# Performance work log

Hardware: AMD Instinct MI355X
Metric: run time of the kernel (lower is better)

## Reference

```python
import jax, jax.numpy as jnp
import numpy as np

NUM_EXPERTS = 8
TOP_K = 2
D_MODEL = 1024
EXPERT_CAP = 512  # dim_feedforward // num_experts = 4096 // 8
B, S = 4, 2048


def setup_inputs() -> dict:
    key = jax.random.key(0)
    ks = jax.random.split(key, 4)
    scale = 1.0 / np.sqrt(D_MODEL)
    x = jax.random.normal(ks[0], (B, S, D_MODEL), dtype=jnp.float32)
    gate_w = jax.random.normal(ks[1], (D_MODEL, NUM_EXPERTS), dtype=jnp.float32) * scale
    w1 = jax.random.normal(ks[2], (NUM_EXPERTS, D_MODEL, EXPERT_CAP), dtype=jnp.float32) * scale
    b1 = jnp.zeros((NUM_EXPERTS, EXPERT_CAP), dtype=jnp.float32)
    w2 = jax.random.normal(ks[3], (NUM_EXPERTS, EXPERT_CAP, D_MODEL), dtype=jnp.float32) * (1.0 / np.sqrt(EXPERT_CAP))
    b2 = jnp.zeros((NUM_EXPERTS, D_MODEL), dtype=jnp.float32)
    return {"x": x, "gate_w": gate_w, "w1": w1, "b1": b1, "w2": w2, "b2": b2}


def reference(x, gate_w, w1, b1, w2, b2):
    Bx, Sx, D = x.shape
    xt = x.reshape(-1, D)  # [N, D], N = B*S
    gates = jax.nn.softmax(xt @ gate_w, axis=-1)           # [N, E]
    topk_g, topk_i = jax.lax.top_k(gates, TOP_K)           # [N, K]
    # Faithful to source: every selected expert is scaled by the SUM of all top-k gates
    tok_w = topk_g.sum(axis=-1)                            # [N]
    sel = (topk_i[:, :, None] == jnp.arange(NUM_EXPERTS)[None, None, :]).any(axis=1)  # [N, E] bool
    # Dense per-expert MLP (E small), then mask-combine (scatter-add equivalent)
    h = jax.nn.gelu(jnp.einsum('nd,edh->enh', xt, w1) + b1[:, None, :], approximate=False)  # [E, N, H]
    y = jnp.einsum('enh,ehd->end', h, w2) + b2[:, None, :]  # [E, N, D]
    out = jnp.einsum('end,ne,n->nd', y, sel.astype(x.dtype), tok_w)  # [N, D]
    return out.reshape(Bx, Sx, D)
```

## Files before the change

### kernel.cpp

```cpp
#include <hip/hip_runtime.h>
#include <math.h>

#define N_TOK 8192
#define DM 1024
#define NE 8
#define HE 512
#define NPAIR 16384
#define MAXMB 264

#define BM 64
#define BN 128
#define BK 64

#define GSTR 1028

typedef __bf16 bf16x8 __attribute__((ext_vector_type(8)));
typedef float f32x4 __attribute__((ext_vector_type(4)));

#define GLOBAL_AS __attribute__((address_space(1)))
#define LDS_AS    __attribute__((address_space(3)))

__device__ __forceinline__ void gl_lds16(const void* g, void* lds) {
    __builtin_amdgcn_global_load_lds((const GLOBAL_AS unsigned int*)g,
                                     (LDS_AS unsigned int*)lds, 16, 0, 0);
}

__device__ __forceinline__ unsigned short f2bf(float f) {
    unsigned int u = __float_as_uint(f);
    u += 0x7fffu + ((u >> 16) & 1u);
    return (unsigned short)(u >> 16);
}

__device__ __forceinline__ float bf2f(unsigned short u) {
    return __uint_as_float(((unsigned int)u) << 16);
}

__device__ __forceinline__ float gelu_exact(float v) {
    return 0.5f * v * (1.0f + erff(v * 0.70710678118654752440f));
}

__device__ __forceinline__ double shfl_xor_dbl(double v, int m) {
    long long l = __double_as_longlong(v);
    int lo = (int)(l & 0xffffffffll);
    int hi = (int)(l >> 32);
    lo = __shfl_xor(lo, m, 64);
    hi = __shfl_xor(hi, m, 64);
    return __longlong_as_double(((long long)hi << 32) | (unsigned long long)(unsigned int)lo);
}

__global__ void transpose_cast2_kernel(const float* __restrict__ w1,
                                       const float* __restrict__ w2,
                                       unsigned short* __restrict__ w1t,
                                       unsigned short* __restrict__ w2t) {
    __shared__ float tile[64][65];
    int z = blockIdx.z;
    const float* src; unsigned short* dst; int R, C, c0, r0;
    if (z < 8) {
        src = w1 + (size_t)z * DM * HE; dst = w1t + (size_t)z * DM * HE;
        R = DM; C = HE; c0 = blockIdx.x * 64; r0 = blockIdx.y * 64;
    } else {
        int e = z - 8;
        src = w2 + (size_t)e * HE * DM; dst = w2t + (size_t)e * HE * DM;
        R = HE; C = DM; c0 = blockIdx.y * 64; r0 = blockIdx.x * 64;
    }
    int tc = threadIdx.x & 63, tg = threadIdx.x >> 6;
    #pragma unroll
    for (int i = 0; i < 16; i++) {
        int r = tg * 16 + i;
        tile[r][tc] = src[(size_t)(r0 + r) * C + (c0 + tc)];
    }
    __syncthreads();
    #pragma unroll
    for (int i = 0; i < 16; i++) {
        int r = tg * 16 + i;
        dst[(size_t)(c0 + r) * R + (r0 + tc)] = f2bf(tile[tc][r]);
    }
}

__global__ __launch_bounds__(256) void gate_cast_kernel(
        const float* __restrict__ x, const float* __restrict__ gw,
        unsigned short* __restrict__ xb,
        float* __restrict__ w_tok, int* __restrict__ e_sel) {
    __shared__ float gls[NE * GSTR];
    int tid = threadIdx.x;
    for (int v = tid; v < 2048; v += 256) {
        float4 g4 = ((const float4*)gw)[v];
        int idx = v * 4;
        int d = idx >> 3;
        int e0 = idx & 7;
        gls[(e0    ) * GSTR + d] = g4.x;
        gls[(e0 + 1) * GSTR + d] = g4.y;
        gls[(e0 + 2) * GSTR + d] = g4.z;
        gls[(e0 + 3) * GSTR + d] = g4.w;
    }
    __syncthreads();

    int n = blockIdx.x * 4 + (tid >> 6);
    int lane = tid & 63;
    const float4* xr = (const float4*)(x + (size_t)n * DM);
    ushort4* xw = (ushort4*)(xb + (size_t)n * DM);

    double s[NE];
    #pragma unroll
    for (int e = 0; e < NE; e++) s[e] = 0.0;

    #pragma unroll
    for (int i = 0; i < 4; i++) {
        float4 x4 = xr[i * 64 + lane];
        ushort4 o;
        o.x = f2bf(x4.x); o.y = f2bf(x4.y); o.z = f2bf(x4.z); o.w = f2bf(x4.w);
        xw[i * 64 + lane] = o;
        int d = (i * 64 + lane) * 4;
        #pragma unroll
        for (int e = 0; e < NE; e++) {
            float4 g4 = *(const float4*)(&gls[e * GSTR + d]);
            s[e] += (double)x4.x * (double)g4.x + (double)x4.y * (double)g4.y
                  + (double)x4.z * (double)g4.z + (double)x4.w * (double)g4.w;
        }
    }
    #pragma unroll
    for (int e = 0; e < NE; e++) {
        for (int off = 32; off > 0; off >>= 1)
            s[e] += shfl_xor_dbl(s[e], off);
    }
    if (lane == 0) {
        double m = s[0];
        for (int e = 1; e < NE; e++) if (s[e] > m) m = s[e];
        double sum = 0.0;
        for (int e = 0; e < NE; e++) sum += exp(s[e] - m);
        int i1 = 0; double v1 = s[0];
        for (int e = 1; e < NE; e++) if (s[e] > v1) { v1 = s[e]; i1 = e; }
        int i2 = -1; double v2 = -1e300;
        for (int e = 0; e < NE; e++) if (e != i1 && s[e] > v2) { v2 = s[e]; i2 = e; }
        w_tok[n] = (float)((exp(v1 - m) + exp(v2 - m)) / sum);
        e_sel[2 * n]     = i1;
        e_sel[2 * n + 1] = i2;
    }
}

__global__ __launch_bounds__(1024) void route_kernel(
        const int* __restrict__ e_sel, int* __restrict__ cnt, int* __restrict__ offs,
        int* __restrict__ pair_tok, int* __restrict__ slotmap,
        int* __restrict__ mb_e, int* __restrict__ mb_base, int* __restrict__ n_mb) {
    __shared__ int wbin[16][NE];
    __shared__ int wstart[16][NE];
    __shared__ int etot[NE], eoffs[NE], bofs[NE];
    int tid = threadIdx.x;
    int w = tid >> 6, l = tid & 63;
    if (l < NE) wbin[w][l] = 0;
    __syncthreads();

    int sel[16];
    #pragma unroll
    for (int k = 0; k < 16; k++) {
        sel[k] = e_sel[tid * 16 + k];
        atomicAdd(&wbin[w][sel[k]], 1);
    }
    __syncthreads();

    if (tid < NE) {
        int t = 0;
        for (int ww = 0; ww < 16; ww++) t += wbin[ww][tid];
        etot[tid] = t;
    }
    __syncthreads();
    if (tid == 0) {
        int a = 0, b = 0;
        for (int e = 0; e < NE; e++) {
            eoffs[e] = a; a += etot[e];
            bofs[e] = b;  b += (etot[e] + BM - 1) / BM;
        }
        n_mb[0] = b;
    }
    __syncthreads();
    if (tid < NE) {
        cnt[tid] = etot[tid];
        offs[tid] = eoffs[tid];
        int r = eoffs[tid];
        for (int ww = 0; ww < 16; ww++) { wstart[ww][tid] = r; r += wbin[ww][tid]; }
        int nb = (etot[tid] + BM - 1) / BM;
        int b0 = bofs[tid];
        for (int b = 0; b < nb; b++) {
            mb_e[b0 + b] = tid;
            mb_base[b0 + b] = eoffs[tid] + b * BM;
        }
    }
    __syncthreads();
    if (l < NE) wbin[w][l] = wstart[w][l];
    __syncthreads();

    #pragma unroll
    for (int k = 0; k < 16; k++) {
        int i = tid * 16 + k;
        int slot = atomicAdd(&wbin[w][sel[k]], 1);
        pair_tok[slot] = i >> 1;
        slotmap[i] = slot;
    }
}

__global__ __launch_bounds__(256, 4) void gemm1_kernel(
        const unsigned short* __restrict__ xb,
        const unsigned short* __restrict__ w1t,
        const float* __restrict__ b1,
        const int* __restrict__ pair_tok,
        const int* __restrict__ cnt, const int* __restrict__ offs,
        const int* __restrict__ mb_e, const int* __restrict__ mb_base,
        const int* __restrict__ n_mb,
        unsigned short* __restrict__ hbuf) {
    int mb = blockIdx.y;
    if (mb >= n_mb[0]) return;
    int e = mb_e[mb];
    int sbase = mb_base[mb];
    int vlim = offs[e] + cnt[e];
    int n0 = blockIdx.x * BN;

    __shared__ __align__(16) unsigned short As[BM * BK];
    __shared__ __align__(16) unsigned short Bs[BN * BK];

    int tid = threadIdx.x;
    int lane = tid & 63;
    int w = tid >> 6;
    int wu = __builtin_amdgcn_readfirstlane(w);
    int l3 = lane >> 3, l7 = lane & 7;
    int g = l7 ^ l3;

    const char* aptr[2];
    const char* bptr[4];
    #pragma unroll
    for (int j = 0; j < 2; j++) {
        int row = w * 16 + j * 8 + l3;
        int slot = sbase + row;
        int t = pair_tok[slot < vlim ? slot : vlim - 1];
        aptr[j] = (const char*)xb + (size_t)t * (DM * 2) + g * 16;
    }
    #pragma unroll
    for (int j = 0; j < 4; j++) {
        int row = w * 32 + j * 8 + l3;
        bptr[j] = (const char*)w1t + ((size_t)e * HE + n0 + row) * (DM * 2) + g * 16;
    }

    int wm = (w & 1) * 32;
    int wn = (w >> 1) * 64;
    int fr = lane & 15;
    int fq = lane >> 4;

    f32x4 acc[2][4];
    #pragma unroll
    for (int i = 0; i < 2; i++)
        #pragma unroll
        for (int j = 0; j < 4; j++)
            acc[i][j] = (f32x4){0.f, 0.f, 0.f, 0.f};

    for (int k0 = 0; k0 < DM; k0 += BK) {
        int kb = k0 * 2;
        #pragma unroll
        for (int j = 0; j < 2; j++)
            gl_lds16(aptr[j] + kb, (char*)As + wu * 2048 + j * 1024);
        #pragma unroll
        for (int j = 0; j < 4; j++)
            gl_lds16(bptr[j] + kb, (char*)Bs + wu * 4096 + j * 1024);
        __syncthreads();
        #pragma unroll
        for (int kk2 = 0; kk2 < 2; kk2++) {
            int sw = ((kk2 * 4 + fq) ^ (fr & 7)) << 4;
            bf16x8 af[2], bfv[4];
            #pragma unroll
            for (int i = 0; i < 2; i++)
                af[i] = *(const bf16x8*)((const char*)As + (wm + i * 16 + fr) * 128 + sw);
            #pragma unroll
            for (int j = 0; j < 4; j++)
                bfv[j] = *(const bf16x8*)((const char*)Bs + (wn + j * 16 + fr) * 128 + sw);
            #pragma unroll
            for (int i = 0; i < 2; i++)
                #pragma unroll
                for (int j = 0; j < 4; j++)
                    acc[i][j] = __builtin_amdgcn_mfma_f32_16x16x32_bf16(af[i], bfv[j], acc[i][j], 0, 0, 0);
        }
        __syncthreads();
    }

    #pragma unroll
    for (int j = 0; j < 4; j++) {
        int nn = n0 + wn + j * 16 + fr;
        float bias = b1[e * HE + nn];
        #pragma unroll
        for (int i = 0; i < 2; i++) {
            #pragma unroll
            for (int r = 0; r < 4; r++) {
                int mm = wm + i * 16 + fq * 4 + r;
                if (sbase + mm < vlim) {
                    float v = acc[i][j][r] + bias;
                    hbuf[(size_t)(sbase + mm) * HE + nn] = f2bf(gelu_exact(v));
                }
            }
        }
    }
}

__global__ __launch_bounds__(256, 4) void gemm2_kernel(
        const unsigned short* __restrict__ hbuf,
        const unsigned short* __restrict__ w2t,
        const float* __restrict__ b2,
        const int* __restrict__ pair_tok,
        const float* __restrict__ w_tok,
        const int* __restrict__ cnt, const int* __restrict__ offs,
        const int* __restrict__ mb_e, const int* __restrict__ mb_base,
        const int* __restrict__ n_mb,
        unsigned short* __restrict__ ybuf) {
    int mb = blockIdx.y;
    if (mb >= n_mb[0]) return;
    int e = mb_e[mb];
    int sbase = mb_base[mb];
    int vlim = offs[e] + cnt[e];
    int n0 = blockIdx.x * BN;

    __shared__ __align__(16) unsigned short As[BM * BK];
    __shared__ __align__(16) unsigned short Bs[BN * BK];
    __shared__ float wts[BM];

    int tid = threadIdx.x;
    if (tid < BM) {
        int slot = sbase + tid;
        wts[tid] = w_tok[pair_tok[slot < vlim ? slot : vlim - 1]];
    }
    __syncthreads();

    int lane = tid & 63;
    int w = tid >> 6;
    int wu = __builtin_amdgcn_readfirstlane(w);
    int l3 = lane >> 3, l7 = lane & 7;
    int g = l7 ^ l3;

    const char* aptr[2];
    const char* bptr[4];
    #pragma unroll
    for (int j = 0; j < 2; j++) {
        int row = w * 16 + j * 8 + l3;
        int slot = sbase + row;
        int cs = (slot < vlim) ? slot : vlim - 1;
        aptr[j] = (const char*)hbuf + (size_t)cs * (HE * 2) + g * 16;
    }
    #pragma unroll
    for (int j = 0; j < 4; j++) {
        int row = w * 32 + j * 8 + l3;
        bptr[j] = (const char*)w2t + ((size_t)e * DM + n0 + row) * (HE * 2) + g * 16;
    }

    int wm = (w & 1) * 32;
    int wn = (w >> 1) * 64;
    int fr = lane & 15;
    int fq = lane >> 4;

    f32x4 acc[2][4];
    #pragma unroll
    for (int i = 0; i < 2; i++)
        #pragma unroll
        for (int j = 0; j < 4; j++)
            acc[i][j] = (f32x4){0.f, 0.f, 0.f, 0.f};

    for (int k0 = 0; k0 < HE; k0 += BK) {
        int kb = k0 * 2;
        #pragma unroll
        for (int j = 0; j < 2; j++)
            gl_lds16(aptr[j] + kb, (char*)As + wu * 2048 + j * 1024);
        #pragma unroll
        for (int j = 0; j < 4; j++)
            gl_lds16(bptr[j] + kb, (char*)Bs + wu * 4096 + j * 1024);
        __syncthreads();
        #pragma unroll
        for (int kk2 = 0; kk2 < 2; kk2++) {
            int sw = ((kk2 * 4 + fq) ^ (fr & 7)) << 4;
            bf16x8 af[2], bfv[4];
            #pragma unroll
            for (int i = 0; i < 2; i++)
                af[i] = *(const bf16x8*)((const char*)As + (wm + i * 16 + fr) * 128 + sw);
            #pragma unroll
            for (int j = 0; j < 4; j++)
                bfv[j] = *(const bf16x8*)((const char*)Bs + (wn + j * 16 + fr) * 128 + sw);
            #pragma unroll
            for (int i = 0; i < 2; i++)
                #pragma unroll
                for (int j = 0; j < 4; j++)
                    acc[i][j] = __builtin_amdgcn_mfma_f32_16x16x32_bf16(af[i], bfv[j], acc[i][j], 0, 0, 0);
        }
        __syncthreads();
    }

    #pragma unroll
    for (int j = 0; j < 4; j++) {
        int dd = n0 + wn + j * 16 + fr;
        float bias = b2[e * DM + dd];
        #pragma unroll
        for (int i = 0; i < 2; i++) {
            #pragma unroll
            for (int r = 0; r < 4; r++) {
                int mm = wm + i * 16 + fq * 4 + r;
                if (sbase + mm < vlim) {
                    float wgt = wts[mm];
                    ybuf[(size_t)(sbase + mm) * DM + dd] = f2bf(wgt * (acc[i][j][r] + bias));
                }
            }
        }
    }
}

__global__ void combine_kernel(const unsigned short* __restrict__ yb,
                               const int* __restrict__ slotmap,
                               float* __restrict__ out) {
    int i = blockIdx.x * 256 + threadIdx.x;
    int n = i >> 8;
    int c = (i & 255) * 4;
    int s1 = slotmap[2 * n];
    int s2 = slotmap[2 * n + 1];
    ushort4 a = *(const ushort4*)(&yb[(size_t)s1 * DM + c]);
    ushort4 b = *(const ushort4*)(&yb[(size_t)s2 * DM + c]);
    float4 o;
    o.x = bf2f(a.x) + bf2f(b.x);
    o.y = bf2f(a.y) + bf2f(b.y);
    o.z = bf2f(a.z) + bf2f(b.z);
    o.w = bf2f(a.w) + bf2f(b.w);
    ((float4*)out)[i] = o;
}

extern "C" void kernel_launch(void* const* d_in, const int* in_sizes, int n_in,
                              void* d_out, int out_size, void* d_ws, size_t ws_size,
                              hipStream_t stream) {
    const float* x  = (const float*)d_in[0];
    const float* gw = (const float*)d_in[1];
    const float* w1 = (const float*)d_in[2];
    const float* b1 = (const float*)d_in[3];
    const float* w2 = (const float*)d_in[4];
    const float* b2 = (const float*)d_in[5];
    float* out = (float*)d_out;

    char* ws = (char*)d_ws;
    unsigned short* ybuf = (unsigned short*)(ws);
    unsigned short* xb   = (unsigned short*)(ws);
    unsigned short* w1t  = (unsigned short*)(ws + 16777216);
    unsigned short* w2t  = (unsigned short*)(ws + 33554432);
    unsigned short* hbuf = (unsigned short*)(ws + 41943040);
    float* w_tok         = (float*)(ws + 58720256);
    int*   e_sel         = (int*)(ws + 58753024);
    int*   slotmap       = (int*)(ws + 58818560);
    int*   cnt           = (int*)(ws + 58884096);
    int*   offs          = (int*)(ws + 58884128);
    int*   pair_tok      = (int*)(ws + 58884224);
    int*   mb_e          = (int*)(ws + 58949760);
    int*   mb_base       = (int*)(ws + 58950848);
    int*   n_mb          = (int*)(ws + 58951936);

    transpose_cast2_kernel<<<dim3(8, 16, 16), 256, 0, stream>>>(w1, w2, w1t, w2t);
    gate_cast_kernel<<<N_TOK / 4, 256, 0, stream>>>(x, gw, xb, w_tok, e_sel);
    route_kernel<<<1, 1024, 0, stream>>>(e_sel, cnt, offs, pair_tok, slotmap,
                                         mb_e, mb_base, n_mb);
    gemm1_kernel<<<dim3(HE / BN, MAXMB), 256, 0, stream>>>(
        xb, w1t, b1, pair_tok, cnt, offs, mb_e, mb_base, n_mb, hbuf);
    gemm2_kernel<<<dim3(DM / BN, MAXMB), 256, 0, stream>>>(
        hbuf, w2t, b2, pair_tok, w_tok, cnt, offs, mb_e, mb_base, n_mb, ybuf);
    combine_kernel<<<(N_TOK * DM / 4) / 256, 256, 0, stream>>>(ybuf, slotmap, out);
}
```

Before: 235.3 us.

## Merge prep kernels, stage GEMM epilogues through LDS, widen combine loads

Folds the weight transpose/cast and the gate/cast kernels into a single launch, so one launch overhead goes away and the two kinds of work can share the GPU. Both GEMM epilogues now write bf16 results into LDS and then store whole rows with 16-byte vector writes, replacing scattered 2-byte global stores. The combine kernel reads 8 bf16 per load instead of 4. The cost is an extra LDS round trip and barrier per tile, plus a merged kernel that uses the larger shared-memory allocation for every block.

```diff
diff --git a/kernel.cpp b/kernel.cpp
--- a/kernel.cpp
+++ b/kernel.cpp
@@ -11,6 +11,7 @@
 #define BM 64
 #define BN 128
 #define BK 64
+#define OSTR 136
 
 #define GSTR 1028
 
@@ -29,10 +30,6 @@
     unsigned int u = __float_as_uint(f);
     u += 0x7fffu + ((u >> 16) & 1u);
     return (unsigned short)(u >> 16);
-}
-
-__device__ __forceinline__ float bf2f(unsigned short u) {
-    return __uint_as_float(((unsigned int)u) << 16);
 }
 
 __device__ __forceinline__ float gelu_exact(float v) {
@@ -48,41 +45,47 @@
     return __longlong_as_double(((long long)hi << 32) | (unsigned long long)(unsigned int)lo);
 }
 
-__global__ void transpose_cast2_kernel(const float* __restrict__ w1,
-                                       const float* __restrict__ w2,
-                                       unsigned short* __restrict__ w1t,
-                                       unsigned short* __restrict__ w2t) {
-    __shared__ float tile[64][65];
-    int z = blockIdx.z;
-    const float* src; unsigned short* dst; int R, C, c0, r0;
-    if (z < 8) {
-        src = w1 + (size_t)z * DM * HE; dst = w1t + (size_t)z * DM * HE;
-        R = DM; C = HE; c0 = blockIdx.x * 64; r0 = blockIdx.y * 64;
-    } else {
-        int e = z - 8;
-        src = w2 + (size_t)e * HE * DM; dst = w2t + (size_t)e * HE * DM;
-        R = HE; C = DM; c0 = blockIdx.y * 64; r0 = blockIdx.x * 64;
-    }
-    int tc = threadIdx.x & 63, tg = threadIdx.x >> 6;
-    #pragma unroll
-    for (int i = 0; i < 16; i++) {
-        int r = tg * 16 + i;
-        tile[r][tc] = src[(size_t)(r0 + r) * C + (c0 + tc)];
-    }
-    __syncthreads();
-    #pragma unroll
-    for (int i = 0; i < 16; i++) {
-        int r = tg * 16 + i;
-        dst[(size_t)(c0 + r) * R + (r0 + tc)] = f2bf(tile[tc][r]);
-    }
-}
-
-__global__ __launch_bounds__(256) void gate_cast_kernel(
+__global__ __launch_bounds__(256) void prep_kernel(
         const float* __restrict__ x, const float* __restrict__ gw,
+        const float* __restrict__ w1, const float* __restrict__ w2,
         unsigned short* __restrict__ xb,
+        unsigned short* __restrict__ w1t, unsigned short* __restrict__ w2t,
         float* __restrict__ w_tok, int* __restrict__ e_sel) {
-    __shared__ float gls[NE * GSTR];
+    __shared__ float smf[NE * GSTR];
+    int bid = blockIdx.x;
     int tid = threadIdx.x;
+
+    if (bid >= 2048) {
+        int t = bid - 2048;
+        int z = t >> 7;
+        int idx = t & 127;
+        int bx = idx & 7, by = idx >> 3;
+        const float* src; unsigned short* dst; int R, C, c0, r0;
+        if (z < 8) {
+            src = w1 + (size_t)z * DM * HE; dst = w1t + (size_t)z * DM * HE;
+            R = DM; C = HE; c0 = bx * 64; r0 = by * 64;
+        } else {
+            int e = z - 8;
+            src = w2 + (size_t)e * HE * DM; dst = w2t + (size_t)e * HE * DM;
+            R = HE; C = DM; c0 = by * 64; r0 = bx * 64;
+        }
+        float (*tile)[65] = (float(*)[65])smf;
+        int tc = tid & 63, tg = tid >> 6;
+        #pragma unroll
+        for (int i = 0; i < 16; i++) {
+            int r = tg * 16 + i;
+            tile[r][tc] = src[(size_t)(r0 + r) * C + (c0 + tc)];
+        }
+        __syncthreads();
+        #pragma unroll
+        for (int i = 0; i < 16; i++) {
+            int r = tg * 16 + i;
+            dst[(size_t)(c0 + r) * R + (r0 + tc)] = f2bf(tile[tc][r]);
+        }
+        return;
+    }
+
+    float* gls = smf;
     for (int v = tid; v < 2048; v += 256) {
         float4 g4 = ((const float4*)gw)[v];
         int idx = v * 4;
@@ -95,7 +98,7 @@
     }
     __syncthreads();
 
-    int n = blockIdx.x * 4 + (tid >> 6);
+    int n = bid * 4 + (tid >> 6);
     int lane = tid & 63;
     const float4* xr = (const float4*)(x + (size_t)n * DM);
     ushort4* xw = (ushort4*)(xb + (size_t)n * DM);
@@ -214,8 +217,9 @@
     int vlim = offs[e] + cnt[e];
     int n0 = blockIdx.x * BN;
 
-    __shared__ __align__(16) unsigned short As[BM * BK];
-    __shared__ __align__(16) unsigned short Bs[BN * BK];
+    __shared__ __align__(16) unsigned short smem[BM * BK + BN * BK];
+    char* As = (char*)smem;
+    char* Bs = (char*)smem + 8192;
 
     int tid = threadIdx.x;
     int lane = tid & 63;
@@ -255,10 +259,10 @@
         int kb = k0 * 2;
         #pragma unroll
         for (int j = 0; j < 2; j++)
-            gl_lds16(aptr[j] + kb, (char*)As + wu * 2048 + j * 1024);
+            gl_lds16(aptr[j] + kb, As + wu * 2048 + j * 1024);
         #pragma unroll
         for (int j = 0; j < 4; j++)
-            gl_lds16(bptr[j] + kb, (char*)Bs + wu * 4096 + j * 1024);
+            gl_lds16(bptr[j] + kb, Bs + wu * 4096 + j * 1024);
         __syncthreads();
         #pragma unroll
         for (int kk2 = 0; kk2 < 2; kk2++) {
@@ -266,10 +270,10 @@
             bf16x8 af[2], bfv[4];
             #pragma unroll
             for (int i = 0; i < 2; i++)
-                af[i] = *(const bf16x8*)((const char*)As + (wm + i * 16 + fr) * 128 + sw);
+                af[i] = *(const bf16x8*)(As + (wm + i * 16 + fr) * 128 + sw);
             #pragma unroll
             for (int j = 0; j < 4; j++)
-                bfv[j] = *(const bf16x8*)((const char*)Bs + (wn + j * 16 + fr) * 128 + sw);
+                bfv[j] = *(const bf16x8*)(Bs + (wn + j * 16 + fr) * 128 + sw);
             #pragma unroll
             for (int i = 0; i < 2; i++)
                 #pragma unroll
@@ -279,21 +283,27 @@
         __syncthreads();
     }
 
+    unsigned short* ot = smem;
     #pragma unroll
     for (int j = 0; j < 4; j++) {
-        int nn = n0 + wn + j * 16 + fr;
-        float bias = b1[e * HE + nn];
+        int nl = wn + j * 16 + fr;
+        float bias = b1[e * HE + n0 + nl];
         #pragma unroll
         for (int i = 0; i < 2; i++) {
             #pragma unroll
             for (int r = 0; r < 4; r++) {
                 int mm = wm + i * 16 + fq * 4 + r;
-                if (sbase + mm < vlim) {
-                    float v = acc[i][j][r] + bias;
-                    hbuf[(size_t)(sbase + mm) * HE + nn] = f2bf(gelu_exact(v));
-                }
+                ot[mm * OSTR + nl] = f2bf(gelu_exact(acc[i][j][r] + bias));
             }
         }
+    }
+    __syncthreads();
+    int row = tid >> 2;
+    int c0 = (tid & 3) * 32;
+    if (sbase + row < vlim) {
+        const uint4* sp = (const uint4*)(ot + row * OSTR + c0);
+        uint4* dp = (uint4*)(hbuf + (size_t)(sbase + row) * HE + n0 + c0);
+        dp[0] = sp[0]; dp[1] = sp[1]; dp[2] = sp[2]; dp[3] = sp[3];
     }
 }
 
@@ -314,8 +324,9 @@
     int vlim = offs[e] + cnt[e];
     int n0 = blockIdx.x * BN;
 
-    __shared__ __align__(16) unsigned short As[BM * BK];
-    __shared__ __align__(16) unsigned short Bs[BN * BK];
+    __shared__ __align__(16) unsigned short smem[BM * BK + BN * BK];
+    char* As = (char*)smem;
+    char* Bs = (char*)smem + 8192;
     __shared__ float wts[BM];
 
     int tid = threadIdx.x;
@@ -362,10 +373,10 @@
         int kb = k0 * 2;
         #pragma unroll
         for (int j = 0; j < 2; j++)
-            gl_lds16(aptr[j] + kb, (char*)As + wu * 2048 + j * 1024);
+            gl_lds16(aptr[j] + kb, As + wu * 2048 + j * 1024);
         #pragma unroll
         for (int j = 0; j < 4; j++)
-            gl_lds16(bptr[j] + kb, (char*)Bs + wu * 4096 + j * 1024);
+            gl_lds16(bptr[j] + kb, Bs + wu * 4096 + j * 1024);
         __syncthreads();
         #pragma unroll
         for (int kk2 = 0; kk2 < 2; kk2++) {
@@ -373,10 +384,10 @@
             bf16x8 af[2], bfv[4];
             #pragma unroll
             for (int i = 0; i < 2; i++)
-                af[i] = *(const bf16x8*)((const char*)As + (wm + i * 16 + fr) * 128 + sw);
+                af[i] = *(const bf16x8*)(As + (wm + i * 16 + fr) * 128 + sw);
             #pragma unroll
             for (int j = 0; j < 4; j++)
-                bfv[j] = *(const bf16x8*)((const char*)Bs + (wn + j * 16 + fr) * 128 + sw);
+                bfv[j] = *(const bf16x8*)(Bs + (wn + j * 16 + fr) * 128 + sw);
             #pragma unroll
             for (int i = 0; i < 2; i++)
                 #pragma unroll
@@ -386,40 +397,54 @@
         __syncthreads();
     }
 
+    unsigned short* ot = smem;
     #pragma unroll
     for (int j = 0; j < 4; j++) {
-        int dd = n0 + wn + j * 16 + fr;
-        float bias = b2[e * DM + dd];
+        int nl = wn + j * 16 + fr;
+        float bias = b2[e * DM + n0 + nl];
         #pragma unroll
         for (int i = 0; i < 2; i++) {
             #pragma unroll
             for (int r = 0; r < 4; r++) {
                 int mm = wm + i * 16 + fq * 4 + r;
-                if (sbase + mm < vlim) {
-                    float wgt = wts[mm];
-                    ybuf[(size_t)(sbase + mm) * DM + dd] = f2bf(wgt * (acc[i][j][r] + bias));
-                }
+                ot[mm * OSTR + nl] = f2bf(wts[mm] * (acc[i][j][r] + bias));
             }
         }
     }
+    __syncthreads();
+    int row = tid >> 2;
+    int c0 = (tid & 3) * 32;
+    if (sbase + row < vlim) {
+        const uint4* sp = (const uint4*)(ot + row * OSTR + c0);
+        uint4* dp = (uint4*)(ybuf + (size_t)(sbase + row) * DM + n0 + c0);
+        dp[0] = sp[0]; dp[1] = sp[1]; dp[2] = sp[2]; dp[3] = sp[3];
+    }
+}
+
+__device__ __forceinline__ float2 bfpair(unsigned int u) {
+    float2 f;
+    f.x = __uint_as_float(u << 16);
+    f.y = __uint_as_float(u & 0xffff0000u);
+    return f;
 }
 
 __global__ void combine_kernel(const unsigned short* __restrict__ yb,
                                const int* __restrict__ slotmap,
                                float* __restrict__ out) {
     int i = blockIdx.x * 256 + threadIdx.x;
-    int n = i >> 8;
-    int c = (i & 255) * 4;
+    int n = i >> 7;
+    int c = (i & 127) * 8;
     int s1 = slotmap[2 * n];
     int s2 = slotmap[2 * n + 1];
-    ushort4 a = *(const ushort4*)(&yb[(size_t)s1 * DM + c]);
-    ushort4 b = *(const ushort4*)(&yb[(size_t)s2 * DM + c]);
-    float4 o;
-    o.x = bf2f(a.x) + bf2f(b.x);
-    o.y = bf2f(a.y) + bf2f(b.y);
-    o.z = bf2f(a.z) + bf2f(b.z);
-    o.w = bf2f(a.w) + bf2f(b.w);
-    ((float4*)out)[i] = o;
+    uint4 a = *(const uint4*)(&yb[(size_t)s1 * DM + c]);
+    uint4 b = *(const uint4*)(&yb[(size_t)s2 * DM + c]);
+    float2 ax = bfpair(a.x), ay = bfpair(a.y), az = bfpair(a.z), aw = bfpair(a.w);
+    float2 bx = bfpair(b.x), by = bfpair(b.y), bz = bfpair(b.z), bw = bfpair(b.w);
+    float4 o0, o1;
+    o0.x = ax.x + bx.x; o0.y = ax.y + bx.y; o0.z = ay.x + by.x; o0.w = ay.y + by.y;
+    o1.x = az.x + bz.x; o1.y = az.y + bz.y; o1.z = aw.x + bw.x; o1.w = aw.y + bw.y;
+    float4* dp = (float4*)(out + (size_t)n * DM + c);
+    dp[0] = o0; dp[1] = o1;
 }
 
 extern "C" void kernel_launch(void* const* d_in, const int* in_sizes, int n_in,
@@ -449,13 +474,12 @@
     int*   mb_base       = (int*)(ws + 58950848);
     int*   n_mb          = (int*)(ws + 58951936);
 
-    transpose_cast2_kernel<<<dim3(8, 16, 16), 256, 0, stream>>>(w1, w2, w1t, w2t);
-    gate_cast_kernel<<<N_TOK / 4, 256, 0, stream>>>(x, gw, xb, w_tok, e_sel);
+    prep_kernel<<<4096, 256, 0, stream>>>(x, gw, w1, w2, xb, w1t, w2t, w_tok, e_sel);
     route_kernel<<<1, 1024, 0, stream>>>(e_sel, cnt, offs, pair_tok, slotmap,
                                          mb_e, mb_base, n_mb);
     gemm1_kernel<<<dim3(HE / BN, MAXMB), 256, 0, stream>>>(
         xb, w1t, b1, pair_tok, cnt, offs, mb_e, mb_base, n_mb, hbuf);
     gemm2_kernel<<<dim3(DM / BN, MAXMB), 256, 0, stream>>>(
         hbuf, w2t, b2, pair_tok, w_tok, cnt, offs, mb_e, mb_base, n_mb, ybuf);
-    combine_kernel<<<(N_TOK * DM / 4) / 256, 256, 0, stream>>>(ybuf, slotmap, out);
-}
+    combine_kernel<<<(N_TOK * DM / 8) / 256, 256, 0, stream>>>(ybuf, slotmap, out);
+}
```

After: 222.0 us. -5.7%, faster.
